# Kernel tuning notes

Hardware: AMD Instinct MI355X
Metric: run time of the kernel (lower is better)

Reference implementation:

```python
import jax, jax.numpy as jnp
import numpy as np

B, S, E, H = 4, 2048, 1024, 16
D = E // H  # head_dim = 64


def setup_inputs() -> dict:
    key = jax.random.key(0)
    ks = jax.random.split(key, 7)
    scale = 1.0 / np.sqrt(E)
    inp = {
        "query": jax.random.normal(ks[0], (B, S, E), jnp.float32),
        "key": jax.random.normal(ks[1], (B, S, E), jnp.float32),
        "value": jax.random.normal(ks[2], (B, S, E), jnp.float32),
        # nn.Linear weights: [out_features, in_features]
        "Wq": jax.random.normal(ks[3], (E, E), jnp.float32) * scale,
        "Wk": jax.random.normal(ks[4], (E, E), jnp.float32) * scale,
        "Wv": jax.random.normal(ks[5], (E, E), jnp.float32) * scale,
        "Wo": jax.random.normal(ks[6], (E, E), jnp.float32) * scale,
        # broadcastable causal mask; masked_fill where mask == 0
        "mask": jnp.tril(jnp.ones((S, S), jnp.bool_))[None, None, :, :],
    }
    return inp


def reference(query, key, value, Wq, Wk, Wv, Wo, mask):
    # projections (Linear, no bias): x @ W.T
    Q = (query @ Wq.T).reshape(B, S, H, D)
    K = (key @ Wk.T).reshape(B, S, H, D)
    V = (value @ Wv.T).reshape(B, S, H, D)
    # full score matrix [B,H,S,S]
    scores = jnp.einsum("bqhd,bkhd->bhqk", Q, K) / jnp.sqrt(jnp.float32(D))
    scores = jnp.where(mask, scores, jnp.float32(-1e20))
    attn = jax.nn.softmax(scores, axis=-1)
    out = jnp.einsum("bhqk,bkhd->bqhd", attn, V).reshape(B, S, E)
    return out @ Wo.T
```

## Files before the change

### kernel.cpp

```cpp
#include <hip/hip_runtime.h>
#include <stdint.h>


#define LOG2E 1.44269504088896340736f

typedef __bf16 bf16;
typedef __attribute__((ext_vector_type(8))) __bf16 bf16x8;
typedef __attribute__((ext_vector_type(4))) __bf16 bf16x4;
typedef __attribute__((ext_vector_type(4))) float f32x4;

static constexpr int Sq = 2048, Eq = 1024;

__device__ __forceinline__ f32x4 mfma16(bf16x8 a, bf16x8 b, f32x4 c) {
  return __builtin_amdgcn_mfma_f32_16x16x32_bf16(a, b, c, 0, 0, 0);
}

__device__ __forceinline__ float fexp2(float x) {
  return __builtin_amdgcn_exp2f(x);
}

__device__ __forceinline__ void gload16(const bf16* g, bf16* l) {
  __builtin_amdgcn_global_load_lds(
      (const __attribute__((address_space(1))) void*)g,
      (__attribute__((address_space(3))) void*)l, 16, 0, 0);
}

__device__ __forceinline__ bf16x8 scale8(bf16x8 v, float s) {
  bf16x8 o;
#pragma unroll
  for (int i = 0; i < 8; ++i) o[i] = (bf16)((float)v[i] * s);
  return o;
}

__device__ __forceinline__ void store4(bf16* p, f32x4 a, float s) {
  bf16x4 v;
#pragma unroll
  for (int rg = 0; rg < 4; ++rg) v[rg] = (bf16)(a[rg] * s);
  *(bf16x4*)p = v;
}

__device__ __forceinline__ bf16x8 cvt8(const float4& a, const float4& b) {
  bf16x8 v;
  v[0] = (bf16)a.x; v[1] = (bf16)a.y; v[2] = (bf16)a.z; v[3] = (bf16)a.w;
  v[4] = (bf16)b.x; v[5] = (bf16)b.y; v[6] = (bf16)b.z; v[7] = (bf16)b.w;
  return v;
}

__global__ void cast_w4(const float* __restrict__ a, const float* __restrict__ b,
                        const float* __restrict__ c, const float* __restrict__ d,
                        bf16* __restrict__ oa, bf16* __restrict__ ob,
                        bf16* __restrict__ oc, bf16* __restrict__ od) {
  int i = blockIdx.x * blockDim.x + threadIdx.x;
  int sel = i >> 17, off = i & ((1 << 17) - 1);
  const float* src = sel == 0 ? a : sel == 1 ? b : sel == 2 ? c : d;
  bf16* dst = sel == 0 ? oa : sel == 1 ? ob : sel == 2 ? oc : od;
  const float4* p = (const float4*)src;
  ((bf16x8*)dst)[off] = cvt8(p[off * 2], p[off * 2 + 1]);
}

__global__ __launch_bounds__(256) void gemm_qkv(
    const float* __restrict__ Aq, const float* __restrict__ Ak,
    const float* __restrict__ Av, const bf16* __restrict__ Wq,
    const bf16* __restrict__ Wk, const bf16* __restrict__ Wv,
    bf16* __restrict__ Qp, bf16* __restrict__ Kp, bf16* __restrict__ Vt) {
  __shared__ __align__(16) bf16 Alds[128 * 64];
  __shared__ __align__(16) bf16 Blds[128 * 64];

  int bid = blockIdx.x;
  int which = bid >> 9;
  int sub = bid & 511;
  const float* Af = which == 0 ? Aq : which == 1 ? Ak : Av;
  const bf16* W = which == 0 ? Wq : which == 1 ? Wk : Wv;

  int wg = (sub & 7) * 64 + (sub >> 3);
  int tm = wg >> 3, tn = wg & 7;
  int tid = threadIdx.x;
  int l = tid & 63, wv = tid >> 6;
  int wm = wv >> 1, wn = wv & 1;
  int l15 = l & 15, lg = l >> 4;

  f32x4 acc[4][4] = {};
  const size_t arow = (size_t)tm * 128, brow = (size_t)tn * 128;

  for (int k0 = 0; k0 < 1024; k0 += 64) {
#pragma unroll
    for (int j = 0; j < 4; ++j) {
      int loc = tid * 16 + j * 4096;
      int r = loc >> 7;
      int c = (loc & 127) >> 1;
      gload16(W + (brow + r) * 1024 + k0 + c, (bf16*)((char*)Blds + loc));
    }
#pragma unroll
    for (int j = 0; j < 4; ++j) {
      int row = (tid >> 3) + j * 32;
      int colf = (tid & 7) * 8;
      const float4* ap = (const float4*)(Af + (arow + row) * 1024 + k0 + colf);
      float4 a0 = ap[0], a1 = ap[1];
      *(bf16x8*)(Alds + row * 64 + colf) = cvt8(a0, a1);
    }
    __syncthreads();
#pragma unroll
    for (int kk = 0; kk < 2; ++kk) {
      bf16x8 af[4], bfr[4];
#pragma unroll
      for (int t = 0; t < 4; ++t) {
        int ma = wm * 64 + t * 16 + l15;
        af[t] = *(const bf16x8*)((const char*)Alds + ma * 128 + 16 * lg + 64 * kk);
        int nb = wn * 64 + t * 16 + l15;
        bfr[t] = *(const bf16x8*)((const char*)Blds + nb * 128 + 16 * lg + 64 * kk);
      }
#pragma unroll
      for (int mt = 0; mt < 4; ++mt)
#pragma unroll
        for (int nt = 0; nt < 4; ++nt)
          acc[mt][nt] = mfma16(af[mt], bfr[nt], acc[mt][nt]);
    }
    __syncthreads();
  }

  int mbase = tm * 128 + wm * 64;
  int nbase = tn * 128 + wn * 64;
  if (which < 2) {
    bf16* C = which == 0 ? Qp : Kp;
#pragma unroll
    for (int mt = 0; mt < 4; ++mt)
#pragma unroll
      for (int nt = 0; nt < 4; ++nt) {
        int m0 = mbase + mt * 16 + (lg << 2);
        int n = nbase + nt * 16 + l15;
#pragma unroll
        for (int rg = 0; rg < 4; ++rg)
          C[(size_t)(m0 + rg) * 1024 + n] = (bf16)acc[mt][nt][rg];
      }
  } else {
#pragma unroll
    for (int mt = 0; mt < 4; ++mt)
#pragma unroll
      for (int nt = 0; nt < 4; ++nt) {
        int m0 = mbase + mt * 16 + (lg << 2);
        int n = nbase + nt * 16 + l15;
        bf16x4 vv;
#pragma unroll
        for (int rg = 0; rg < 4; ++rg) vv[rg] = (bf16)acc[mt][nt][rg];
        int bb = m0 >> 11, s0 = m0 & 2047;
        int sp = (s0 & ~31) | (((s0 >> 4) & 1) << 2) | (((s0 >> 2) & 3) << 3);
        size_t off =
            ((size_t)((bb * 16 + (n >> 6)) * 64 + (n & 63))) * 2048 + sp;
        *(bf16x4*)(Vt + off) = vv;
      }
  }
}

template <int MODE, int AFP32>
__global__ __launch_bounds__(256) void gemm_bt(const void* __restrict__ Ain,
                                               const bf16* __restrict__ W,
                                               void* __restrict__ Cout) {
  __shared__ __align__(16) bf16 Alds[128 * 64];
  __shared__ __align__(16) bf16 Blds[128 * 64];

  int bid = blockIdx.x;
  int nwg = gridDim.x;
  int wg = (bid & 7) * (nwg >> 3) + (bid >> 3);
  int tm = wg >> 3, tn = wg & 7;
  int tid = threadIdx.x;
  int l = tid & 63, wv = tid >> 6;
  int wm = wv >> 1, wn = wv & 1;
  int l15 = l & 15, lg = l >> 4;

  f32x4 acc[4][4] = {};
  const size_t arow = (size_t)tm * 128, brow = (size_t)tn * 128;
  const bf16* Ab = (const bf16*)Ain;
  const float* Af = (const float*)Ain;

  for (int k0 = 0; k0 < 1024; k0 += 64) {
#pragma unroll
    for (int j = 0; j < 4; ++j) {
      int loc = tid * 16 + j * 4096;
      int r = loc >> 7;
      int c = (loc & 127) >> 1;
      gload16(W + (brow + r) * 1024 + k0 + c, (bf16*)((char*)Blds + loc));
      if (!AFP32)
        gload16(Ab + (arow + r) * 1024 + k0 + c, (bf16*)((char*)Alds + loc));
    }
    if (AFP32) {
#pragma unroll
      for (int j = 0; j < 4; ++j) {
        int row = (tid >> 3) + j * 32;
        int colf = (tid & 7) * 8;
        const float4* ap = (const float4*)(Af + (arow + row) * 1024 + k0 + colf);
        float4 a0 = ap[0], a1 = ap[1];
        *(bf16x8*)(Alds + row * 64 + colf) = cvt8(a0, a1);
      }
    }
    __syncthreads();
#pragma unroll
    for (int kk = 0; kk < 2; ++kk) {
      bf16x8 af[4], bfr[4];
#pragma unroll
      for (int t = 0; t < 4; ++t) {
        int ma = wm * 64 + t * 16 + l15;
        af[t] = *(const bf16x8*)((const char*)Alds + ma * 128 + 16 * lg + 64 * kk);
        int nb = wn * 64 + t * 16 + l15;
        bfr[t] = *(const bf16x8*)((const char*)Blds + nb * 128 + 16 * lg + 64 * kk);
      }
#pragma unroll
      for (int mt = 0; mt < 4; ++mt)
#pragma unroll
        for (int nt = 0; nt < 4; ++nt)
          acc[mt][nt] = mfma16(af[mt], bfr[nt], acc[mt][nt]);
    }
    __syncthreads();
  }

  int mbase = tm * 128 + wm * 64;
  int nbase = tn * 128 + wn * 64;
#pragma unroll
  for (int mt = 0; mt < 4; ++mt)
#pragma unroll
    for (int nt = 0; nt < 4; ++nt) {
      int m0 = mbase + mt * 16 + (lg << 2);
      int n = nbase + nt * 16 + l15;
#pragma unroll
      for (int rg = 0; rg < 4; ++rg) {
        if (MODE == 0)
          ((bf16*)Cout)[(size_t)(m0 + rg) * 1024 + n] = (bf16)acc[mt][nt][rg];
        else
          ((float*)Cout)[(size_t)(m0 + rg) * 1024 + n] = acc[mt][nt][rg];
      }
    }
}

__global__ __launch_bounds__(256) void attn_kernel(
    const bf16* __restrict__ Qp, const bf16* __restrict__ Kp,
    const bf16* __restrict__ Vt, bf16* __restrict__ AO) {
  __shared__ __align__(16) bf16 sm[2][2][4096];

  int bid = blockIdx.x;
  int bh = ((bid & 7) << 3) | ((bid >> 3) & 7);
  int j = bid >> 6;
  int b = bh >> 4, h = bh & 15;
  int tid = threadIdx.x;
  int w = tid >> 6, l = tid & 63;
  int l15 = l & 15, lg = l >> 4;

  int ncA = 2 * j + 2, ncB = 32 - 2 * j;
  const float sc = 0.125f * LOG2E;
  bf16 one1 = (bf16)1.0f;
  bf16x8 ones = {one1, one1, one1, one1, one1, one1, one1, one1};

  const bf16* Kbase = Kp + (size_t)(b * 2048) * 1024 + h * 64;
  const bf16* Vbase = Vt + (size_t)(bh * 64) * 2048;

  int qw0 = j * 128 + w * 32;
  int cdiag = 2 * j + (w >> 1);
  int qg0 = qw0 + l15, qg1 = qw0 + 16 + l15;
  const bf16* qp_ = Qp + (size_t)(b * 2048 + qw0 + l15) * 1024 + h * 64 + 8 * lg;
  bf16x8 q00 = scale8(*(const bf16x8*)qp_, sc);
  bf16x8 q01 = scale8(*(const bf16x8*)(qp_ + 32), sc);
  bf16x8 q10 = scale8(*(const bf16x8*)(qp_ + 16384), sc);
  bf16x8 q11 = scale8(*(const bf16x8*)(qp_ + 16384 + 32), sc);

  f32x4 r0 = {0.f, 0.f, 0.f, 0.f}, r1 = r0;
  f32x4 o0[4] = {}, o1[4] = {};

#define STAGE(c_, bufp)                                                     \
  do {                                                                      \
    int _c = (c_);                                                          \
    _Pragma("unroll") for (int jj = 0; jj < 2; ++jj) {                      \
      int loc = tid * 16 + jj * 4096;                                       \
      int row = loc >> 7, u = (loc >> 4) & 7;                               \
      int sel = (u ^ (row & 7)) << 3;                                       \
      gload16(Kbase + (size_t)(_c * 64 + row) * 1024 + sel,                 \
              (bf16*)((char*)sm[bufp][0] + loc));                           \
      gload16(Vbase + (size_t)row * 2048 + _c * 64 + sel,                   \
              (bf16*)((char*)sm[bufp][1] + loc));                           \
    }                                                                       \
  } while (0)

#define CHUNKC(c_)                                                          \
  do {                                                                      \
    const int _c = (c_);                                                    \
    const char* lK = (const char*)sm[cur][0];                               \
    const char* lV = (const char*)sm[cur][1];                               \
    const f32x4 cinit = {-6.f, -6.f, -6.f, -6.f};                           \
    f32x4 s0[4], s1[4];                                                     \
    _Pragma("unroll") for (int kt = 0; kt < 4; ++kt) {                      \
      int row = kt * 16 + l15, sw = (row & 7) << 4;                         \
      const char* kb = lK + row * 128;                                      \
      bf16x8 kf0 = *(const bf16x8*)(kb + ((lg * 16) ^ sw));                 \
      bf16x8 kf1 = *(const bf16x8*)(kb + ((64 + lg * 16) ^ sw));            \
      s0[kt] = mfma16(kf1, q01, mfma16(kf0, q00, cinit));                   \
      s1[kt] = mfma16(kf1, q11, mfma16(kf0, q10, cinit));                   \
    }                                                                       \
    if (_c == cdiag) {                                                      \
      _Pragma("unroll") for (int kt = 0; kt < 4; ++kt)                      \
          _Pragma("unroll") for (int rg = 0; rg < 4; ++rg) {                \
        int kg = _c * 64 + kt * 16 + 4 * lg + rg;                           \
        if (kg > qg0) s0[kt][rg] = -1e30f;                                  \
        if (kg > qg1) s1[kt][rg] = -1e30f;                                  \
      }                                                                     \
    }                                                                       \
    bf16x8 plo0, phi0, plo1, phi1;                                          \
    _Pragma("unroll") for (int rg = 0; rg < 4; ++rg) {                      \
      plo0[rg] = (bf16)fexp2(s0[0][rg]); plo0[rg + 4] = (bf16)fexp2(s0[1][rg]); \
      phi0[rg] = (bf16)fexp2(s0[2][rg]); phi0[rg + 4] = (bf16)fexp2(s0[3][rg]); \
      plo1[rg] = (bf16)fexp2(s1[0][rg]); plo1[rg + 4] = (bf16)fexp2(s1[1][rg]); \
      phi1[rg] = (bf16)fexp2(s1[2][rg]); phi1[rg + 4] = (bf16)fexp2(s1[3][rg]); \
    }                                                                       \
    r0 = mfma16(ones, phi0, mfma16(ones, plo0, r0));                        \
    r1 = mfma16(ones, phi1, mfma16(ones, plo1, r1));                        \
    _Pragma("unroll") for (int dt = 0; dt < 4; ++dt) {                      \
      int row = dt * 16 + l15, sw = (row & 7) << 4;                         \
      const char* vb = lV + row * 128;                                      \
      bf16x8 vf0 = *(const bf16x8*)(vb + ((lg * 16) ^ sw));                 \
      bf16x8 vf1 = *(const bf16x8*)(vb + ((64 + lg * 16) ^ sw));            \
      o0[dt] = mfma16(vf1, phi0, mfma16(vf0, plo0, o0[dt]));                \
      o1[dt] = mfma16(vf1, phi1, mfma16(vf0, plo1, o1[dt]));                \
    }                                                                       \
  } while (0)

#define STOREOUT()                                                          \
  do {                                                                      \
    float inv0 = 1.0f / r0[0], inv1 = 1.0f / r1[0];                         \
    bf16* ob = AO + (size_t)(b * 2048 + qw0 + l15) * 1024 + h * 64 + 4 * lg; \
    _Pragma("unroll") for (int dt = 0; dt < 4; ++dt) {                      \
      store4(ob + dt * 16, o0[dt], inv0);                                   \
      store4(ob + 16384 + dt * 16, o1[dt], inv1);                           \
    }                                                                       \
  } while (0)

  STAGE(0, 0);
  __syncthreads();
  int cur = 0;

  for (int c = 0; c < ncA; ++c) {
    int g = c + 1;
    STAGE(g < ncA ? g : g - ncA, cur ^ 1);
    if (c <= cdiag) CHUNKC(c);
    __syncthreads();
    cur ^= 1;
  }
  STOREOUT();

  qw0 = (15 - j) * 128 + w * 32;
  cdiag = 2 * (15 - j) + (w >> 1);
  qg0 = qw0 + l15; qg1 = qw0 + 16 + l15;
  qp_ = Qp + (size_t)(b * 2048 + qw0 + l15) * 1024 + h * 64 + 8 * lg;
  q00 = scale8(*(const bf16x8*)qp_, sc);
  q01 = scale8(*(const bf16x8*)(qp_ + 32), sc);
  q10 = scale8(*(const bf16x8*)(qp_ + 16384), sc);
  q11 = scale8(*(const bf16x8*)(qp_ + 16384 + 32), sc);
  r0 = f32x4{0.f, 0.f, 0.f, 0.f}; r1 = r0;
#pragma unroll
  for (int dt = 0; dt < 4; ++dt) { o0[dt] = r0; o1[dt] = r0; }

  for (int c = 0; c < ncB; ++c) {
    if (c + 1 < ncB) STAGE(c + 1, cur ^ 1);
    if (c <= cdiag) CHUNKC(c);
    __syncthreads();
    cur ^= 1;
  }
  STOREOUT();
#undef STAGE
#undef CHUNKC
#undef STOREOUT
}

extern "C" void kernel_launch(void* const* d_in, const int* in_sizes, int n_in,
                              void* d_out, int out_size, void* d_ws, size_t ws_size,
                              hipStream_t stream) {
  (void)in_sizes; (void)n_in; (void)out_size; (void)ws_size;
  const float* dq = (const float*)d_in[0];
  const float* dk = (const float*)d_in[1];
  const float* dv = (const float*)d_in[2];
  const float* wq = (const float*)d_in[3];
  const float* wk = (const float*)d_in[4];
  const float* wv = (const float*)d_in[5];
  const float* wo = (const float*)d_in[6];

  char* ws = (char*)d_ws;
  const size_t MB = 1u << 20;
  bf16* AO  = (bf16*)(ws + 0 * MB);
  bf16* wqb = (bf16*)(ws + 48 * MB);
  bf16* wkb = (bf16*)(ws + 50 * MB);
  bf16* wvb = (bf16*)(ws + 52 * MB);
  bf16* wob = (bf16*)(ws + 54 * MB);
  bf16* Qp  = (bf16*)(ws + 56 * MB);
  bf16* Kp  = (bf16*)(ws + 72 * MB);
  bf16* Vt  = (bf16*)(ws + 88 * MB);

  cast_w4<<<4 * 512, 256, 0, stream>>>(wq, wk, wv, wo, wqb, wkb, wvb, wob);
  gemm_qkv<<<1536, 256, 0, stream>>>(dq, dk, dv, wqb, wkb, wvb, Qp, Kp, Vt);
  attn_kernel<<<512, 256, 0, stream>>>(Qp, Kp, Vt, AO);
  gemm_bt<2, 0><<<512, 256, 0, stream>>>(AO, wob, d_out);
}
```

Before: 187.3 us.

## Double-buffer fp32-input projection GEMM and split QKV into three launches

The fused QKV projection kernel becomes a templated GEMM with double-buffered LDS. Next-tile fp32 A loads and async B loads are issued before the current tile's MFMAs, and the bf16 conversion is written to LDS after compute. This hides global latency behind math with one barrier per step instead of two. The single 1536-block launch becomes three 512-block launches, adding launch overhead, doubling LDS use (which may lower occupancy) and adding register pressure from holding the prefetched float4s.

```diff
diff --git a/kernel.cpp b/kernel.cpp
--- a/kernel.cpp
+++ b/kernel.cpp
@@ -58,21 +58,15 @@
   ((bf16x8*)dst)[off] = cvt8(p[off * 2], p[off * 2 + 1]);
 }
 
-__global__ __launch_bounds__(256) void gemm_qkv(
-    const float* __restrict__ Aq, const float* __restrict__ Ak,
-    const float* __restrict__ Av, const bf16* __restrict__ Wq,
-    const bf16* __restrict__ Wk, const bf16* __restrict__ Wv,
-    bf16* __restrict__ Qp, bf16* __restrict__ Kp, bf16* __restrict__ Vt) {
-  __shared__ __align__(16) bf16 Alds[128 * 64];
-  __shared__ __align__(16) bf16 Blds[128 * 64];
+template <int MODE>
+__global__ __launch_bounds__(256) void gemm_af32(const float* __restrict__ Af,
+                                                 const bf16* __restrict__ W,
+                                                 bf16* __restrict__ C) {
+  __shared__ __align__(16) bf16 Alds[2][128 * 64];
+  __shared__ __align__(16) bf16 Blds[2][128 * 64];
 
   int bid = blockIdx.x;
-  int which = bid >> 9;
-  int sub = bid & 511;
-  const float* Af = which == 0 ? Aq : which == 1 ? Ak : Av;
-  const bf16* W = which == 0 ? Wq : which == 1 ? Wk : Wv;
-
-  int wg = (sub & 7) * 64 + (sub >> 3);
+  int wg = (bid & 7) * 64 + (bid >> 3);
   int tm = wg >> 3, tn = wg & 7;
   int tid = threadIdx.x;
   int l = tid & 63, wv = tid >> 6;
@@ -81,6 +75,115 @@
 
   f32x4 acc[4][4] = {};
   const size_t arow = (size_t)tm * 128, brow = (size_t)tn * 128;
+  const int arow_t = tid >> 3;
+  const int acol_t = (tid & 7) * 8;
+
+  float4 a0[4], a1[4];
+
+#define ISSUEA(k0_)                                                          \
+  _Pragma("unroll") for (int j = 0; j < 4; ++j) {                            \
+    const float4* ap =                                                       \
+        (const float4*)(Af + (arow + arow_t + j * 32) * 1024 + (k0_) + acol_t); \
+    a0[j] = ap[0]; a1[j] = ap[1];                                            \
+  }
+#define WRITEA(bufp)                                                         \
+  _Pragma("unroll") for (int j = 0; j < 4; ++j) {                            \
+    *(bf16x8*)(Alds[bufp] + (arow_t + j * 32) * 64 + acol_t) =               \
+        cvt8(a0[j], a1[j]);                                                  \
+  }
+#define ISSUEB(k0_, bufp)                                                    \
+  _Pragma("unroll") for (int j = 0; j < 4; ++j) {                            \
+    int loc = tid * 16 + j * 4096;                                           \
+    int r = loc >> 7;                                                        \
+    int c = (loc & 127) >> 1;                                                \
+    gload16(W + (brow + r) * 1024 + (k0_) + c,                               \
+            (bf16*)((char*)Blds[bufp] + loc));                               \
+  }
+
+  ISSUEA(0);
+  ISSUEB(0, 0);
+  WRITEA(0);
+  __syncthreads();
+
+  int cur = 0;
+  for (int step = 0; step < 16; ++step) {
+    if (step < 15) {
+      int k1 = (step + 1) * 64;
+      ISSUEA(k1);
+      ISSUEB(k1, cur ^ 1);
+    }
+#pragma unroll
+    for (int kk = 0; kk < 2; ++kk) {
+      bf16x8 af[4], bfr[4];
+#pragma unroll
+      for (int t = 0; t < 4; ++t) {
+        int ma = wm * 64 + t * 16 + l15;
+        af[t] = *(const bf16x8*)((const char*)Alds[cur] + ma * 128 + 16 * lg + 64 * kk);
+        int nb = wn * 64 + t * 16 + l15;
+        bfr[t] = *(const bf16x8*)((const char*)Blds[cur] + nb * 128 + 16 * lg + 64 * kk);
+      }
+#pragma unroll
+      for (int mt = 0; mt < 4; ++mt)
+#pragma unroll
+        for (int nt = 0; nt < 4; ++nt)
+          acc[mt][nt] = mfma16(af[mt], bfr[nt], acc[mt][nt]);
+    }
+    if (step < 15) WRITEA(cur ^ 1);
+    __syncthreads();
+    cur ^= 1;
+  }
+#undef ISSUEA
+#undef WRITEA
+#undef ISSUEB
+
+  int mbase = tm * 128 + wm * 64;
+  int nbase = tn * 128 + wn * 64;
+  if (MODE == 0) {
+#pragma unroll
+    for (int mt = 0; mt < 4; ++mt)
+#pragma unroll
+      for (int nt = 0; nt < 4; ++nt) {
+        int m0 = mbase + mt * 16 + (lg << 2);
+        int n = nbase + nt * 16 + l15;
+#pragma unroll
+        for (int rg = 0; rg < 4; ++rg)
+          C[(size_t)(m0 + rg) * 1024 + n] = (bf16)acc[mt][nt][rg];
+      }
+  } else {
+#pragma unroll
+    for (int mt = 0; mt < 4; ++mt)
+#pragma unroll
+      for (int nt = 0; nt < 4; ++nt) {
+        int m0 = mbase + mt * 16 + (lg << 2);
+        int n = nbase + nt * 16 + l15;
+        bf16x4 vv;
+#pragma unroll
+        for (int rg = 0; rg < 4; ++rg) vv[rg] = (bf16)acc[mt][nt][rg];
+        int bb = m0 >> 11, s0 = m0 & 2047;
+        int sp = (s0 & ~31) | (((s0 >> 4) & 1) << 2) | (((s0 >> 2) & 3) << 3);
+        size_t off =
+            ((size_t)((bb * 16 + (n >> 6)) * 64 + (n & 63))) * 2048 + sp;
+        *(bf16x4*)(C + off) = vv;
+      }
+  }
+}
+
+__global__ __launch_bounds__(256) void gemm_wo(const bf16* __restrict__ A,
+                                               const bf16* __restrict__ W,
+                                               float* __restrict__ Cout) {
+  __shared__ __align__(16) bf16 Alds[128 * 64];
+  __shared__ __align__(16) bf16 Blds[128 * 64];
+
+  int bid = blockIdx.x;
+  int wg = (bid & 7) * 64 + (bid >> 3);
+  int tm = wg >> 3, tn = wg & 7;
+  int tid = threadIdx.x;
+  int l = tid & 63, wv = tid >> 6;
+  int wm = wv >> 1, wn = wv & 1;
+  int l15 = l & 15, lg = l >> 4;
+
+  f32x4 acc[4][4] = {};
+  const size_t arow = (size_t)tm * 128, brow = (size_t)tn * 128;
 
   for (int k0 = 0; k0 < 1024; k0 += 64) {
 #pragma unroll
@@ -89,14 +192,7 @@
       int r = loc >> 7;
       int c = (loc & 127) >> 1;
       gload16(W + (brow + r) * 1024 + k0 + c, (bf16*)((char*)Blds + loc));
-    }
-#pragma unroll
-    for (int j = 0; j < 4; ++j) {
-      int row = (tid >> 3) + j * 32;
-      int colf = (tid & 7) * 8;
-      const float4* ap = (const float4*)(Af + (arow + row) * 1024 + k0 + colf);
-      float4 a0 = ap[0], a1 = ap[1];
-      *(bf16x8*)(Alds + row * 64 + colf) = cvt8(a0, a1);
+      gload16(A + (arow + r) * 1024 + k0 + c, (bf16*)((char*)Alds + loc));
     }
     __syncthreads();
 #pragma unroll
@@ -120,100 +216,6 @@
 
   int mbase = tm * 128 + wm * 64;
   int nbase = tn * 128 + wn * 64;
-  if (which < 2) {
-    bf16* C = which == 0 ? Qp : Kp;
-#pragma unroll
-    for (int mt = 0; mt < 4; ++mt)
-#pragma unroll
-      for (int nt = 0; nt < 4; ++nt) {
-        int m0 = mbase + mt * 16 + (lg << 2);
-        int n = nbase + nt * 16 + l15;
-#pragma unroll
-        for (int rg = 0; rg < 4; ++rg)
-          C[(size_t)(m0 + rg) * 1024 + n] = (bf16)acc[mt][nt][rg];
-      }
-  } else {
-#pragma unroll
-    for (int mt = 0; mt < 4; ++mt)
-#pragma unroll
-      for (int nt = 0; nt < 4; ++nt) {
-        int m0 = mbase + mt * 16 + (lg << 2);
-        int n = nbase + nt * 16 + l15;
-        bf16x4 vv;
-#pragma unroll
-        for (int rg = 0; rg < 4; ++rg) vv[rg] = (bf16)acc[mt][nt][rg];
-        int bb = m0 >> 11, s0 = m0 & 2047;
-        int sp = (s0 & ~31) | (((s0 >> 4) & 1) << 2) | (((s0 >> 2) & 3) << 3);
-        size_t off =
-            ((size_t)((bb * 16 + (n >> 6)) * 64 + (n & 63))) * 2048 + sp;
-        *(bf16x4*)(Vt + off) = vv;
-      }
-  }
-}
-
-template <int MODE, int AFP32>
-__global__ __launch_bounds__(256) void gemm_bt(const void* __restrict__ Ain,
-                                               const bf16* __restrict__ W,
-                                               void* __restrict__ Cout) {
-  __shared__ __align__(16) bf16 Alds[128 * 64];
-  __shared__ __align__(16) bf16 Blds[128 * 64];
-
-  int bid = blockIdx.x;
-  int nwg = gridDim.x;
-  int wg = (bid & 7) * (nwg >> 3) + (bid >> 3);
-  int tm = wg >> 3, tn = wg & 7;
-  int tid = threadIdx.x;
-  int l = tid & 63, wv = tid >> 6;
-  int wm = wv >> 1, wn = wv & 1;
-  int l15 = l & 15, lg = l >> 4;
-
-  f32x4 acc[4][4] = {};
-  const size_t arow = (size_t)tm * 128, brow = (size_t)tn * 128;
-  const bf16* Ab = (const bf16*)Ain;
-  const float* Af = (const float*)Ain;
-
-  for (int k0 = 0; k0 < 1024; k0 += 64) {
-#pragma unroll
-    for (int j = 0; j < 4; ++j) {
-      int loc = tid * 16 + j * 4096;
-      int r = loc >> 7;
-      int c = (loc & 127) >> 1;
-      gload16(W + (brow + r) * 1024 + k0 + c, (bf16*)((char*)Blds + loc));
-      if (!AFP32)
-        gload16(Ab + (arow + r) * 1024 + k0 + c, (bf16*)((char*)Alds + loc));
-    }
-    if (AFP32) {
-#pragma unroll
-      for (int j = 0; j < 4; ++j) {
-        int row = (tid >> 3) + j * 32;
-        int colf = (tid & 7) * 8;
-        const float4* ap = (const float4*)(Af + (arow + row) * 1024 + k0 + colf);
-        float4 a0 = ap[0], a1 = ap[1];
-        *(bf16x8*)(Alds + row * 64 + colf) = cvt8(a0, a1);
-      }
-    }
-    __syncthreads();
-#pragma unroll
-    for (int kk = 0; kk < 2; ++kk) {
-      bf16x8 af[4], bfr[4];
-#pragma unroll
-      for (int t = 0; t < 4; ++t) {
-        int ma = wm * 64 + t * 16 + l15;
-        af[t] = *(const bf16x8*)((const char*)Alds + ma * 128 + 16 * lg + 64 * kk);
-        int nb = wn * 64 + t * 16 + l15;
-        bfr[t] = *(const bf16x8*)((const char*)Blds + nb * 128 + 16 * lg + 64 * kk);
-      }
-#pragma unroll
-      for (int mt = 0; mt < 4; ++mt)
-#pragma unroll
-        for (int nt = 0; nt < 4; ++nt)
-          acc[mt][nt] = mfma16(af[mt], bfr[nt], acc[mt][nt]);
-    }
-    __syncthreads();
-  }
-
-  int mbase = tm * 128 + wm * 64;
-  int nbase = tn * 128 + wn * 64;
 #pragma unroll
   for (int mt = 0; mt < 4; ++mt)
 #pragma unroll
@@ -221,12 +223,8 @@
       int m0 = mbase + mt * 16 + (lg << 2);
       int n = nbase + nt * 16 + l15;
 #pragma unroll
-      for (int rg = 0; rg < 4; ++rg) {
-        if (MODE == 0)
-          ((bf16*)Cout)[(size_t)(m0 + rg) * 1024 + n] = (bf16)acc[mt][nt][rg];
-        else
-          ((float*)Cout)[(size_t)(m0 + rg) * 1024 + n] = acc[mt][nt][rg];
-      }
+      for (int rg = 0; rg < 4; ++rg)
+        Cout[(size_t)(m0 + rg) * 1024 + n] = acc[mt][nt][rg];
     }
 }
 
@@ -390,7 +388,9 @@
   bf16* Vt  = (bf16*)(ws + 88 * MB);
 
   cast_w4<<<4 * 512, 256, 0, stream>>>(wq, wk, wv, wo, wqb, wkb, wvb, wob);
-  gemm_qkv<<<1536, 256, 0, stream>>>(dq, dk, dv, wqb, wkb, wvb, Qp, Kp, Vt);
+  gemm_af32<0><<<512, 256, 0, stream>>>(dq, wqb, Qp);
+  gemm_af32<0><<<512, 256, 0, stream>>>(dk, wkb, Kp);
+  gemm_af32<1><<<512, 256, 0, stream>>>(dv, wvb, Vt);
   attn_kernel<<<512, 256, 0, stream>>>(Qp, Kp, Vt, AO);
-  gemm_bt<2, 0><<<512, 256, 0, stream>>>(AO, wob, d_out);
-}
+  gemm_wo<<<512, 256, 0, stream>>>(AO, wob, (float*)d_out);
+}
```

Result: slower. 216.8 us (+15.8%).

## Triple-buffer attention K/V staging into one fused loop; split QKV projection launches

Applied to the files above, without the earlier changes.

The attention kernel's two separate chunk loops (the causal pair of query tiles) are merged into a single 34-iteration loop. It uses three LDS buffers and a prefetch distance of two, with a raw s_waitcnt vmcnt(4) plus s_barrier replacing __syncthreads. This aims to hide global-to-LDS load latency and drop one barrier drain at the seam between the two query tiles. The QKV projection is split from one 1536-block launch into three 512-block template launches, and the output GEMM is specialised. The extra LDS buffer raises shared memory per block, and the hand-written vmcnt count depends on how many loads STAGE issues per thread.

```diff
diff --git a/kernel.cpp b/kernel.cpp
--- a/kernel.cpp
+++ b/kernel.cpp
@@ -58,21 +58,15 @@
   ((bf16x8*)dst)[off] = cvt8(p[off * 2], p[off * 2 + 1]);
 }
 
-__global__ __launch_bounds__(256) void gemm_qkv(
-    const float* __restrict__ Aq, const float* __restrict__ Ak,
-    const float* __restrict__ Av, const bf16* __restrict__ Wq,
-    const bf16* __restrict__ Wk, const bf16* __restrict__ Wv,
-    bf16* __restrict__ Qp, bf16* __restrict__ Kp, bf16* __restrict__ Vt) {
+template <int MODE>
+__global__ __launch_bounds__(256) void gemm_proj(const float* __restrict__ Af,
+                                                 const bf16* __restrict__ W,
+                                                 bf16* __restrict__ C) {
   __shared__ __align__(16) bf16 Alds[128 * 64];
   __shared__ __align__(16) bf16 Blds[128 * 64];
 
   int bid = blockIdx.x;
-  int which = bid >> 9;
-  int sub = bid & 511;
-  const float* Af = which == 0 ? Aq : which == 1 ? Ak : Av;
-  const bf16* W = which == 0 ? Wq : which == 1 ? Wk : Wv;
-
-  int wg = (sub & 7) * 64 + (sub >> 3);
+  int wg = (bid & 7) * 64 + (bid >> 3);
   int tm = wg >> 3, tn = wg & 7;
   int tid = threadIdx.x;
   int l = tid & 63, wv = tid >> 6;
@@ -120,8 +114,7 @@
 
   int mbase = tm * 128 + wm * 64;
   int nbase = tn * 128 + wn * 64;
-  if (which < 2) {
-    bf16* C = which == 0 ? Qp : Kp;
+  if (MODE == 0) {
 #pragma unroll
     for (int mt = 0; mt < 4; ++mt)
 #pragma unroll
@@ -146,21 +139,19 @@
         int sp = (s0 & ~31) | (((s0 >> 4) & 1) << 2) | (((s0 >> 2) & 3) << 3);
         size_t off =
             ((size_t)((bb * 16 + (n >> 6)) * 64 + (n & 63))) * 2048 + sp;
-        *(bf16x4*)(Vt + off) = vv;
+        *(bf16x4*)(C + off) = vv;
       }
   }
 }
 
-template <int MODE, int AFP32>
-__global__ __launch_bounds__(256) void gemm_bt(const void* __restrict__ Ain,
+__global__ __launch_bounds__(256) void gemm_wo(const bf16* __restrict__ A,
                                                const bf16* __restrict__ W,
-                                               void* __restrict__ Cout) {
+                                               float* __restrict__ Cout) {
   __shared__ __align__(16) bf16 Alds[128 * 64];
   __shared__ __align__(16) bf16 Blds[128 * 64];
 
   int bid = blockIdx.x;
-  int nwg = gridDim.x;
-  int wg = (bid & 7) * (nwg >> 3) + (bid >> 3);
+  int wg = (bid & 7) * 64 + (bid >> 3);
   int tm = wg >> 3, tn = wg & 7;
   int tid = threadIdx.x;
   int l = tid & 63, wv = tid >> 6;
@@ -169,8 +160,6 @@
 
   f32x4 acc[4][4] = {};
   const size_t arow = (size_t)tm * 128, brow = (size_t)tn * 128;
-  const bf16* Ab = (const bf16*)Ain;
-  const float* Af = (const float*)Ain;
 
   for (int k0 = 0; k0 < 1024; k0 += 64) {
 #pragma unroll
@@ -179,18 +168,7 @@
       int r = loc >> 7;
       int c = (loc & 127) >> 1;
       gload16(W + (brow + r) * 1024 + k0 + c, (bf16*)((char*)Blds + loc));
-      if (!AFP32)
-        gload16(Ab + (arow + r) * 1024 + k0 + c, (bf16*)((char*)Alds + loc));
-    }
-    if (AFP32) {
-#pragma unroll
-      for (int j = 0; j < 4; ++j) {
-        int row = (tid >> 3) + j * 32;
-        int colf = (tid & 7) * 8;
-        const float4* ap = (const float4*)(Af + (arow + row) * 1024 + k0 + colf);
-        float4 a0 = ap[0], a1 = ap[1];
-        *(bf16x8*)(Alds + row * 64 + colf) = cvt8(a0, a1);
-      }
+      gload16(A + (arow + r) * 1024 + k0 + c, (bf16*)((char*)Alds + loc));
     }
     __syncthreads();
 #pragma unroll
@@ -221,19 +199,15 @@
       int m0 = mbase + mt * 16 + (lg << 2);
       int n = nbase + nt * 16 + l15;
 #pragma unroll
-      for (int rg = 0; rg < 4; ++rg) {
-        if (MODE == 0)
-          ((bf16*)Cout)[(size_t)(m0 + rg) * 1024 + n] = (bf16)acc[mt][nt][rg];
-        else
-          ((float*)Cout)[(size_t)(m0 + rg) * 1024 + n] = acc[mt][nt][rg];
-      }
+      for (int rg = 0; rg < 4; ++rg)
+        Cout[(size_t)(m0 + rg) * 1024 + n] = acc[mt][nt][rg];
     }
 }
 
 __global__ __launch_bounds__(256) void attn_kernel(
     const bf16* __restrict__ Qp, const bf16* __restrict__ Kp,
     const bf16* __restrict__ Vt, bf16* __restrict__ AO) {
-  __shared__ __align__(16) bf16 sm[2][2][4096];
+  __shared__ __align__(16) bf16 sm[3][2][4096];
 
   int bid = blockIdx.x;
   int bh = ((bid & 7) << 3) | ((bid >> 3) & 7);
@@ -243,7 +217,8 @@
   int w = tid >> 6, l = tid & 63;
   int l15 = l & 15, lg = l >> 4;
 
-  int ncA = 2 * j + 2, ncB = 32 - 2 * j;
+  const int ncA = 2 * j + 2;
+  const int NC = 34;
   const float sc = 0.125f * LOG2E;
   bf16 one1 = (bf16)1.0f;
   bf16x8 ones = {one1, one1, one1, one1, one1, one1, one1, one1};
@@ -277,11 +252,11 @@
     }                                                                       \
   } while (0)
 
-#define CHUNKC(c_)                                                          \
+#define CHUNKC(c_, bufc_)                                                   \
   do {                                                                      \
     const int _c = (c_);                                                    \
-    const char* lK = (const char*)sm[cur][0];                               \
-    const char* lV = (const char*)sm[cur][1];                               \
+    const char* lK = (const char*)sm[bufc_][0];                             \
+    const char* lV = (const char*)sm[bufc_][1];                             \
     const f32x4 cinit = {-6.f, -6.f, -6.f, -6.f};                           \
     f32x4 s0[4], s1[4];                                                     \
     _Pragma("unroll") for (int kt = 0; kt < 4; ++kt) {                      \
@@ -330,35 +305,37 @@
   } while (0)
 
   STAGE(0, 0);
-  __syncthreads();
-  int cur = 0;
-
-  for (int c = 0; c < ncA; ++c) {
-    int g = c + 1;
-    STAGE(g < ncA ? g : g - ncA, cur ^ 1);
-    if (c <= cdiag) CHUNKC(c);
-    __syncthreads();
-    cur ^= 1;
-  }
-  STOREOUT();
-
-  qw0 = (15 - j) * 128 + w * 32;
-  cdiag = 2 * (15 - j) + (w >> 1);
-  qg0 = qw0 + l15; qg1 = qw0 + 16 + l15;
-  qp_ = Qp + (size_t)(b * 2048 + qw0 + l15) * 1024 + h * 64 + 8 * lg;
-  q00 = scale8(*(const bf16x8*)qp_, sc);
-  q01 = scale8(*(const bf16x8*)(qp_ + 32), sc);
-  q10 = scale8(*(const bf16x8*)(qp_ + 16384), sc);
-  q11 = scale8(*(const bf16x8*)(qp_ + 16384 + 32), sc);
-  r0 = f32x4{0.f, 0.f, 0.f, 0.f}; r1 = r0;
-#pragma unroll
-  for (int dt = 0; dt < 4; ++dt) { o0[dt] = r0; o1[dt] = r0; }
-
-  for (int c = 0; c < ncB; ++c) {
-    if (c + 1 < ncB) STAGE(c + 1, cur ^ 1);
-    if (c <= cdiag) CHUNKC(c);
-    __syncthreads();
-    cur ^= 1;
+  STAGE(1, 1);
+
+  for (int g = 0; g < NC; ++g) {
+    if (g < NC - 1)
+      asm volatile("s_waitcnt vmcnt(4)\n\ts_barrier" ::: "memory");
+    else
+      asm volatile("s_waitcnt vmcnt(0)\n\ts_barrier" ::: "memory");
+
+    if (g + 2 < NC) {
+      int gn = g + 2;
+      int cn = gn < ncA ? gn : gn - ncA;
+      STAGE(cn, gn % 3);
+    }
+
+    if (g == ncA) {
+      STOREOUT();
+      qw0 = (15 - j) * 128 + w * 32;
+      cdiag = 2 * (15 - j) + (w >> 1);
+      qg0 = qw0 + l15; qg1 = qw0 + 16 + l15;
+      qp_ = Qp + (size_t)(b * 2048 + qw0 + l15) * 1024 + h * 64 + 8 * lg;
+      q00 = scale8(*(const bf16x8*)qp_, sc);
+      q01 = scale8(*(const bf16x8*)(qp_ + 32), sc);
+      q10 = scale8(*(const bf16x8*)(qp_ + 16384), sc);
+      q11 = scale8(*(const bf16x8*)(qp_ + 16384 + 32), sc);
+      r0 = f32x4{0.f, 0.f, 0.f, 0.f}; r1 = r0;
+#pragma unroll
+      for (int dt = 0; dt < 4; ++dt) { o0[dt] = r0; o1[dt] = r0; }
+    }
+
+    int c = g < ncA ? g : g - ncA;
+    if (c <= cdiag) CHUNKC(c, g % 3);
   }
   STOREOUT();
 #undef STAGE
@@ -390,7 +367,9 @@
   bf16* Vt  = (bf16*)(ws + 88 * MB);
 
   cast_w4<<<4 * 512, 256, 0, stream>>>(wq, wk, wv, wo, wqb, wkb, wvb, wob);
-  gemm_qkv<<<1536, 256, 0, stream>>>(dq, dk, dv, wqb, wkb, wvb, Qp, Kp, Vt);
+  gemm_proj<0><<<512, 256, 0, stream>>>(dq, wqb, Qp);
+  gemm_proj<0><<<512, 256, 0, stream>>>(dk, wkb, Kp);
+  gemm_proj<1><<<512, 256, 0, stream>>>(dv, wvb, Vt);
   attn_kernel<<<512, 256, 0, stream>>>(Qp, Kp, Vt, AO);
-  gemm_bt<2, 0><<<512, 256, 0, stream>>>(AO, wob, d_out);
-}
+  gemm_wo<<<512, 256, 0, stream>>>(AO, wob, (float*)d_out);
+}
```

Result: no change. 190.7 us (+1.8%).

## Split QKV GEMM into three launches, halve N tile, regrid attention to 64-row pairs

Applied to the files above, without the earlier changes.

The fused QKV projection kernel is replaced by three separate launches of a generic GEMM whose N tile shrinks from 128 to 64, doubling the block count to 1024 per GEMM. The attention kernel now gives each wave 16 query rows instead of 32 and runs 1024 blocks. Each block pairs a short causal tile with its complement in a single loop over 33 chunks, so every block does the same amount of work. The aim is more blocks and more even load across CUs, at the cost of less reuse of each staged K/V or weight tile per MFMA, two extra launches and more redundant global loads.

```diff
diff --git a/kernel.cpp b/kernel.cpp
--- a/kernel.cpp
+++ b/kernel.cpp
@@ -58,129 +58,32 @@
   ((bf16x8*)dst)[off] = cvt8(p[off * 2], p[off * 2 + 1]);
 }
 
-__global__ __launch_bounds__(256) void gemm_qkv(
-    const float* __restrict__ Aq, const float* __restrict__ Ak,
-    const float* __restrict__ Av, const bf16* __restrict__ Wq,
-    const bf16* __restrict__ Wk, const bf16* __restrict__ Wv,
-    bf16* __restrict__ Qp, bf16* __restrict__ Kp, bf16* __restrict__ Vt) {
+template <int MODE, int AFP32>
+__global__ __launch_bounds__(256) void gemm_t(const void* __restrict__ Ain,
+                                              const bf16* __restrict__ W,
+                                              void* __restrict__ Cout) {
   __shared__ __align__(16) bf16 Alds[128 * 64];
-  __shared__ __align__(16) bf16 Blds[128 * 64];
+  __shared__ __align__(16) bf16 Blds[64 * 64];
 
   int bid = blockIdx.x;
-  int which = bid >> 9;
-  int sub = bid & 511;
-  const float* Af = which == 0 ? Aq : which == 1 ? Ak : Av;
-  const bf16* W = which == 0 ? Wq : which == 1 ? Wk : Wv;
-
-  int wg = (sub & 7) * 64 + (sub >> 3);
-  int tm = wg >> 3, tn = wg & 7;
+  int wg = (bid & 7) * 128 + (bid >> 3);
+  int tm = wg >> 4, tn = wg & 15;
   int tid = threadIdx.x;
   int l = tid & 63, wv = tid >> 6;
   int wm = wv >> 1, wn = wv & 1;
   int l15 = l & 15, lg = l >> 4;
 
-  f32x4 acc[4][4] = {};
-  const size_t arow = (size_t)tm * 128, brow = (size_t)tn * 128;
-
-  for (int k0 = 0; k0 < 1024; k0 += 64) {
-#pragma unroll
-    for (int j = 0; j < 4; ++j) {
-      int loc = tid * 16 + j * 4096;
-      int r = loc >> 7;
-      int c = (loc & 127) >> 1;
-      gload16(W + (brow + r) * 1024 + k0 + c, (bf16*)((char*)Blds + loc));
-    }
-#pragma unroll
-    for (int j = 0; j < 4; ++j) {
-      int row = (tid >> 3) + j * 32;
-      int colf = (tid & 7) * 8;
-      const float4* ap = (const float4*)(Af + (arow + row) * 1024 + k0 + colf);
-      float4 a0 = ap[0], a1 = ap[1];
-      *(bf16x8*)(Alds + row * 64 + colf) = cvt8(a0, a1);
-    }
-    __syncthreads();
-#pragma unroll
-    for (int kk = 0; kk < 2; ++kk) {
-      bf16x8 af[4], bfr[4];
-#pragma unroll
-      for (int t = 0; t < 4; ++t) {
-        int ma = wm * 64 + t * 16 + l15;
-        af[t] = *(const bf16x8*)((const char*)Alds + ma * 128 + 16 * lg + 64 * kk);
-        int nb = wn * 64 + t * 16 + l15;
-        bfr[t] = *(const bf16x8*)((const char*)Blds + nb * 128 + 16 * lg + 64 * kk);
-      }
-#pragma unroll
-      for (int mt = 0; mt < 4; ++mt)
-#pragma unroll
-        for (int nt = 0; nt < 4; ++nt)
-          acc[mt][nt] = mfma16(af[mt], bfr[nt], acc[mt][nt]);
-    }
-    __syncthreads();
-  }
-
-  int mbase = tm * 128 + wm * 64;
-  int nbase = tn * 128 + wn * 64;
-  if (which < 2) {
-    bf16* C = which == 0 ? Qp : Kp;
-#pragma unroll
-    for (int mt = 0; mt < 4; ++mt)
-#pragma unroll
-      for (int nt = 0; nt < 4; ++nt) {
-        int m0 = mbase + mt * 16 + (lg << 2);
-        int n = nbase + nt * 16 + l15;
-#pragma unroll
-        for (int rg = 0; rg < 4; ++rg)
-          C[(size_t)(m0 + rg) * 1024 + n] = (bf16)acc[mt][nt][rg];
-      }
-  } else {
-#pragma unroll
-    for (int mt = 0; mt < 4; ++mt)
-#pragma unroll
-      for (int nt = 0; nt < 4; ++nt) {
-        int m0 = mbase + mt * 16 + (lg << 2);
-        int n = nbase + nt * 16 + l15;
-        bf16x4 vv;
-#pragma unroll
-        for (int rg = 0; rg < 4; ++rg) vv[rg] = (bf16)acc[mt][nt][rg];
-        int bb = m0 >> 11, s0 = m0 & 2047;
-        int sp = (s0 & ~31) | (((s0 >> 4) & 1) << 2) | (((s0 >> 2) & 3) << 3);
-        size_t off =
-            ((size_t)((bb * 16 + (n >> 6)) * 64 + (n & 63))) * 2048 + sp;
-        *(bf16x4*)(Vt + off) = vv;
-      }
-  }
-}
-
-template <int MODE, int AFP32>
-__global__ __launch_bounds__(256) void gemm_bt(const void* __restrict__ Ain,
-                                               const bf16* __restrict__ W,
-                                               void* __restrict__ Cout) {
-  __shared__ __align__(16) bf16 Alds[128 * 64];
-  __shared__ __align__(16) bf16 Blds[128 * 64];
-
-  int bid = blockIdx.x;
-  int nwg = gridDim.x;
-  int wg = (bid & 7) * (nwg >> 3) + (bid >> 3);
-  int tm = wg >> 3, tn = wg & 7;
-  int tid = threadIdx.x;
-  int l = tid & 63, wv = tid >> 6;
-  int wm = wv >> 1, wn = wv & 1;
-  int l15 = l & 15, lg = l >> 4;
-
-  f32x4 acc[4][4] = {};
-  const size_t arow = (size_t)tm * 128, brow = (size_t)tn * 128;
+  f32x4 acc[4][2] = {};
+  const size_t arow = (size_t)tm * 128, brow = (size_t)tn * 64;
   const bf16* Ab = (const bf16*)Ain;
   const float* Af = (const float*)Ain;
 
   for (int k0 = 0; k0 < 1024; k0 += 64) {
 #pragma unroll
-    for (int j = 0; j < 4; ++j) {
+    for (int j = 0; j < 2; ++j) {
       int loc = tid * 16 + j * 4096;
-      int r = loc >> 7;
-      int c = (loc & 127) >> 1;
+      int r = loc >> 7, c = (loc & 127) >> 1;
       gload16(W + (brow + r) * 1024 + k0 + c, (bf16*)((char*)Blds + loc));
-      if (!AFP32)
-        gload16(Ab + (arow + r) * 1024 + k0 + c, (bf16*)((char*)Alds + loc));
     }
     if (AFP32) {
 #pragma unroll
@@ -191,43 +94,71 @@
         float4 a0 = ap[0], a1 = ap[1];
         *(bf16x8*)(Alds + row * 64 + colf) = cvt8(a0, a1);
       }
+    } else {
+#pragma unroll
+      for (int j = 0; j < 4; ++j) {
+        int loc = tid * 16 + j * 4096;
+        int r = loc >> 7, c = (loc & 127) >> 1;
+        gload16(Ab + (arow + r) * 1024 + k0 + c, (bf16*)((char*)Alds + loc));
+      }
     }
     __syncthreads();
 #pragma unroll
     for (int kk = 0; kk < 2; ++kk) {
-      bf16x8 af[4], bfr[4];
+      bf16x8 af[4], bfr[2];
 #pragma unroll
       for (int t = 0; t < 4; ++t) {
         int ma = wm * 64 + t * 16 + l15;
         af[t] = *(const bf16x8*)((const char*)Alds + ma * 128 + 16 * lg + 64 * kk);
-        int nb = wn * 64 + t * 16 + l15;
+      }
+#pragma unroll
+      for (int t = 0; t < 2; ++t) {
+        int nb = wn * 32 + t * 16 + l15;
         bfr[t] = *(const bf16x8*)((const char*)Blds + nb * 128 + 16 * lg + 64 * kk);
       }
 #pragma unroll
       for (int mt = 0; mt < 4; ++mt)
 #pragma unroll
-        for (int nt = 0; nt < 4; ++nt)
+        for (int nt = 0; nt < 2; ++nt)
           acc[mt][nt] = mfma16(af[mt], bfr[nt], acc[mt][nt]);
     }
     __syncthreads();
   }
 
   int mbase = tm * 128 + wm * 64;
-  int nbase = tn * 128 + wn * 64;
-#pragma unroll
-  for (int mt = 0; mt < 4; ++mt)
-#pragma unroll
-    for (int nt = 0; nt < 4; ++nt) {
-      int m0 = mbase + mt * 16 + (lg << 2);
-      int n = nbase + nt * 16 + l15;
-#pragma unroll
-      for (int rg = 0; rg < 4; ++rg) {
-        if (MODE == 0)
-          ((bf16*)Cout)[(size_t)(m0 + rg) * 1024 + n] = (bf16)acc[mt][nt][rg];
-        else
-          ((float*)Cout)[(size_t)(m0 + rg) * 1024 + n] = acc[mt][nt][rg];
-      }
-    }
+  int nbase = tn * 64 + wn * 32;
+  if (MODE == 0 || MODE == 2) {
+#pragma unroll
+    for (int mt = 0; mt < 4; ++mt)
+#pragma unroll
+      for (int nt = 0; nt < 2; ++nt) {
+        int m0 = mbase + mt * 16 + (lg << 2);
+        int n = nbase + nt * 16 + l15;
+#pragma unroll
+        for (int rg = 0; rg < 4; ++rg) {
+          if (MODE == 0)
+            ((bf16*)Cout)[(size_t)(m0 + rg) * 1024 + n] = (bf16)acc[mt][nt][rg];
+          else
+            ((float*)Cout)[(size_t)(m0 + rg) * 1024 + n] = acc[mt][nt][rg];
+        }
+      }
+  } else {
+#pragma unroll
+    for (int mt = 0; mt < 4; ++mt)
+#pragma unroll
+      for (int nt = 0; nt < 2; ++nt) {
+        int m0 = mbase + mt * 16 + (lg << 2);
+        int n = nbase + nt * 16 + l15;
+        bf16x4 vv;
+#pragma unroll
+        for (int rg = 0; rg < 4; ++rg) vv[rg] = (bf16)acc[mt][nt][rg];
+        int bb = m0 >> 11, s0 = m0 & 2047;
+        int sp = (s0 & ~31) | (((s0 >> 4) & 1) << 2) | (((s0 >> 2) & 3) << 3);
+        size_t off =
+            ((size_t)((bb * 16 + (n >> 6)) * 64 + (n & 63))) * 2048 + sp;
+        *(bf16x4*)((bf16*)Cout + off) = vv;
+      }
+  }
 }
 
 __global__ __launch_bounds__(256) void attn_kernel(
@@ -237,13 +168,14 @@
 
   int bid = blockIdx.x;
   int bh = ((bid & 7) << 3) | ((bid >> 3) & 7);
-  int j = bid >> 6;
+  int t = bid >> 6;
   int b = bh >> 4, h = bh & 15;
   int tid = threadIdx.x;
   int w = tid >> 6, l = tid & 63;
   int l15 = l & 15, lg = l >> 4;
 
-  int ncA = 2 * j + 2, ncB = 32 - 2 * j;
+  const int ncA = t + 1;
+  const int NC = 33;
   const float sc = 0.125f * LOG2E;
   bf16 one1 = (bf16)1.0f;
   bf16x8 ones = {one1, one1, one1, one1, one1, one1, one1, one1};
@@ -251,17 +183,13 @@
   const bf16* Kbase = Kp + (size_t)(b * 2048) * 1024 + h * 64;
   const bf16* Vbase = Vt + (size_t)(bh * 64) * 2048;
 
-  int qw0 = j * 128 + w * 32;
-  int cdiag = 2 * j + (w >> 1);
-  int qg0 = qw0 + l15, qg1 = qw0 + 16 + l15;
+  int qw0 = 64 * t + w * 16;
+  int qg0 = qw0 + l15;
   const bf16* qp_ = Qp + (size_t)(b * 2048 + qw0 + l15) * 1024 + h * 64 + 8 * lg;
   bf16x8 q00 = scale8(*(const bf16x8*)qp_, sc);
   bf16x8 q01 = scale8(*(const bf16x8*)(qp_ + 32), sc);
-  bf16x8 q10 = scale8(*(const bf16x8*)(qp_ + 16384), sc);
-  bf16x8 q11 = scale8(*(const bf16x8*)(qp_ + 16384 + 32), sc);
-
-  f32x4 r0 = {0.f, 0.f, 0.f, 0.f}, r1 = r0;
-  f32x4 o0[4] = {}, o1[4] = {};
+  f32x4 r0 = {0.f, 0.f, 0.f, 0.f};
+  f32x4 o0[4] = {};
 
 #define STAGE(c_, bufp)                                                     \
   do {                                                                      \
@@ -277,86 +205,75 @@
     }                                                                       \
   } while (0)
 
-#define CHUNKC(c_)                                                          \
+#define CHUNKC(c_, last_)                                                   \
   do {                                                                      \
     const int _c = (c_);                                                    \
     const char* lK = (const char*)sm[cur][0];                               \
     const char* lV = (const char*)sm[cur][1];                               \
     const f32x4 cinit = {-6.f, -6.f, -6.f, -6.f};                           \
-    f32x4 s0[4], s1[4];                                                     \
+    f32x4 s[4];                                                             \
     _Pragma("unroll") for (int kt = 0; kt < 4; ++kt) {                      \
       int row = kt * 16 + l15, sw = (row & 7) << 4;                         \
       const char* kb = lK + row * 128;                                      \
       bf16x8 kf0 = *(const bf16x8*)(kb + ((lg * 16) ^ sw));                 \
       bf16x8 kf1 = *(const bf16x8*)(kb + ((64 + lg * 16) ^ sw));            \
-      s0[kt] = mfma16(kf1, q01, mfma16(kf0, q00, cinit));                   \
-      s1[kt] = mfma16(kf1, q11, mfma16(kf0, q10, cinit));                   \
-    }                                                                       \
-    if (_c == cdiag) {                                                      \
+      s[kt] = mfma16(kf1, q01, mfma16(kf0, q00, cinit));                    \
+    }                                                                       \
+    if (last_) {                                                            \
       _Pragma("unroll") for (int kt = 0; kt < 4; ++kt)                      \
           _Pragma("unroll") for (int rg = 0; rg < 4; ++rg) {                \
         int kg = _c * 64 + kt * 16 + 4 * lg + rg;                           \
-        if (kg > qg0) s0[kt][rg] = -1e30f;                                  \
-        if (kg > qg1) s1[kt][rg] = -1e30f;                                  \
+        if (kg > qg0) s[kt][rg] = -1e30f;                                   \
       }                                                                     \
     }                                                                       \
-    bf16x8 plo0, phi0, plo1, phi1;                                          \
+    bf16x8 plo, phi;                                                        \
     _Pragma("unroll") for (int rg = 0; rg < 4; ++rg) {                      \
-      plo0[rg] = (bf16)fexp2(s0[0][rg]); plo0[rg + 4] = (bf16)fexp2(s0[1][rg]); \
-      phi0[rg] = (bf16)fexp2(s0[2][rg]); phi0[rg + 4] = (bf16)fexp2(s0[3][rg]); \
-      plo1[rg] = (bf16)fexp2(s1[0][rg]); plo1[rg + 4] = (bf16)fexp2(s1[1][rg]); \
-      phi1[rg] = (bf16)fexp2(s1[2][rg]); phi1[rg + 4] = (bf16)fexp2(s1[3][rg]); \
-    }                                                                       \
-    r0 = mfma16(ones, phi0, mfma16(ones, plo0, r0));                        \
-    r1 = mfma16(ones, phi1, mfma16(ones, plo1, r1));                        \
+      plo[rg] = (bf16)fexp2(s[0][rg]);                                      \
+      plo[rg + 4] = (bf16)fexp2(s[1][rg]);                                  \
+      phi[rg] = (bf16)fexp2(s[2][rg]);                                      \
+      phi[rg + 4] = (bf16)fexp2(s[3][rg]);                                  \
+    }                                                                       \
+    r0 = mfma16(ones, phi, mfma16(ones, plo, r0));                          \
     _Pragma("unroll") for (int dt = 0; dt < 4; ++dt) {                      \
       int row = dt * 16 + l15, sw = (row & 7) << 4;                         \
       const char* vb = lV + row * 128;                                      \
       bf16x8 vf0 = *(const bf16x8*)(vb + ((lg * 16) ^ sw));                 \
       bf16x8 vf1 = *(const bf16x8*)(vb + ((64 + lg * 16) ^ sw));            \
-      o0[dt] = mfma16(vf1, phi0, mfma16(vf0, plo0, o0[dt]));                \
-      o1[dt] = mfma16(vf1, phi1, mfma16(vf0, plo1, o1[dt]));                \
+      o0[dt] = mfma16(vf1, phi, mfma16(vf0, plo, o0[dt]));                  \
     }                                                                       \
   } while (0)
 
 #define STOREOUT()                                                          \
   do {                                                                      \
-    float inv0 = 1.0f / r0[0], inv1 = 1.0f / r1[0];                         \
+    float inv = 1.0f / r0[0];                                               \
     bf16* ob = AO + (size_t)(b * 2048 + qw0 + l15) * 1024 + h * 64 + 4 * lg; \
-    _Pragma("unroll") for (int dt = 0; dt < 4; ++dt) {                      \
-      store4(ob + dt * 16, o0[dt], inv0);                                   \
-      store4(ob + 16384 + dt * 16, o1[dt], inv1);                           \
-    }                                                                       \
+    _Pragma("unroll") for (int dt = 0; dt < 4; ++dt)                        \
+        store4(ob + dt * 16, o0[dt], inv);                                  \
   } while (0)
 
   STAGE(0, 0);
   __syncthreads();
   int cur = 0;
 
-  for (int c = 0; c < ncA; ++c) {
-    int g = c + 1;
-    STAGE(g < ncA ? g : g - ncA, cur ^ 1);
-    if (c <= cdiag) CHUNKC(c);
-    __syncthreads();
-    cur ^= 1;
-  }
-  STOREOUT();
-
-  qw0 = (15 - j) * 128 + w * 32;
-  cdiag = 2 * (15 - j) + (w >> 1);
-  qg0 = qw0 + l15; qg1 = qw0 + 16 + l15;
-  qp_ = Qp + (size_t)(b * 2048 + qw0 + l15) * 1024 + h * 64 + 8 * lg;
-  q00 = scale8(*(const bf16x8*)qp_, sc);
-  q01 = scale8(*(const bf16x8*)(qp_ + 32), sc);
-  q10 = scale8(*(const bf16x8*)(qp_ + 16384), sc);
-  q11 = scale8(*(const bf16x8*)(qp_ + 16384 + 32), sc);
-  r0 = f32x4{0.f, 0.f, 0.f, 0.f}; r1 = r0;
-#pragma unroll
-  for (int dt = 0; dt < 4; ++dt) { o0[dt] = r0; o1[dt] = r0; }
-
-  for (int c = 0; c < ncB; ++c) {
-    if (c + 1 < ncB) STAGE(c + 1, cur ^ 1);
-    if (c <= cdiag) CHUNKC(c);
+  for (int g = 0; g < NC; ++g) {
+    if (g + 1 < NC) {
+      int gn = g + 1;
+      STAGE(gn < ncA ? gn : gn - ncA, cur ^ 1);
+    }
+    if (g == ncA) {
+      STOREOUT();
+      qw0 = 64 * (31 - t) + w * 16;
+      qg0 = qw0 + l15;
+      qp_ = Qp + (size_t)(b * 2048 + qw0 + l15) * 1024 + h * 64 + 8 * lg;
+      q00 = scale8(*(const bf16x8*)qp_, sc);
+      q01 = scale8(*(const bf16x8*)(qp_ + 32), sc);
+      r0 = f32x4{0.f, 0.f, 0.f, 0.f};
+#pragma unroll
+      for (int dt = 0; dt < 4; ++dt) o0[dt] = r0;
+    }
+    int c = g < ncA ? g : g - ncA;
+    bool last = (g == ncA - 1) || (g == NC - 1);
+    CHUNKC(c, last);
     __syncthreads();
     cur ^= 1;
   }
@@ -390,7 +307,9 @@
   bf16* Vt  = (bf16*)(ws + 88 * MB);
 
   cast_w4<<<4 * 512, 256, 0, stream>>>(wq, wk, wv, wo, wqb, wkb, wvb, wob);
-  gemm_qkv<<<1536, 256, 0, stream>>>(dq, dk, dv, wqb, wkb, wvb, Qp, Kp, Vt);
-  attn_kernel<<<512, 256, 0, stream>>>(Qp, Kp, Vt, AO);
-  gemm_bt<2, 0><<<512, 256, 0, stream>>>(AO, wob, d_out);
-}
+  gemm_t<0, 1><<<1024, 256, 0, stream>>>(dq, wqb, (void*)Qp);
+  gemm_t<0, 1><<<1024, 256, 0, stream>>>(dk, wkb, (void*)Kp);
+  gemm_t<1, 1><<<1024, 256, 0, stream>>>(dv, wvb, (void*)Vt);
+  attn_kernel<<<1024, 256, 0, stream>>>(Qp, Kp, Vt, AO);
+  gemm_t<2, 0><<<1024, 256, 0, stream>>>(AO, wob, d_out);
+}
```

Measured after the change: 208.9 us. 1.12x slower.
